# Performance work log

Measured on AMD Instinct MI355X. Metric: run time of the kernel, lower is better.

## Reference

```python
import jax, jax.numpy as jnp
import numpy as np

NUM_EMBEDDINGS = 1024
LATENT_SIZE = 256
N = 131072


def setup_inputs() -> dict:
    key = jax.random.key(0)
    k1, k2 = jax.random.split(key)
    inputs = jax.random.normal(k1, (N, LATENT_SIZE), dtype=jnp.float32)
    embed = jax.random.normal(k2, (LATENT_SIZE, NUM_EMBEDDINGS), dtype=jnp.float32)
    return {"inputs": inputs, "embed": embed}


def reference(inputs, embed):
    # Squared Euclidean distances: [N, K]
    dist = (
        jnp.sum(inputs * inputs, axis=1, keepdims=True)
        - 2.0 * (inputs @ embed)
        + jnp.sum(embed * embed, axis=0, keepdims=True)
    )
    embed_ind = jnp.argmin(dist, axis=1)  # [N]
    embed_onehot = jax.nn.one_hot(embed_ind, NUM_EMBEDDINGS, dtype=inputs.dtype)  # [N, K]
    # Gather codebook vectors: embedding lookup into embed.T -> [N, D]
    quantize = embed.T[embed_ind]
    # Commitment-style loss (eval path: no EMA buffer updates)
    loss = jnp.mean((jax.lax.stop_gradient(quantize) - inputs) ** 2)
    # Straight-through estimator
    quantize = inputs + jax.lax.stop_gradient(quantize - inputs)
    avg_probs = jnp.mean(embed_onehot, axis=0)  # [K]
    perplexity = jnp.exp(-jnp.sum(avg_probs * jnp.log(avg_probs + 1e-10)))
    return quantize, loss, perplexity, embed_ind
```

## Files before the change

### kernel.cpp

```cpp
#include <hip/hip_runtime.h>
#include <math.h>

#define M_ROWS 131072
#define D_DIM 256
#define NCODES 1024
#define QELEMS (M_ROWS * D_DIM)

#define WS_EMBEDT   0u
#define WS_ENORM    1048576u
#define WS_PARTIALS 1052672u
#define WS_COUNTS   9441280u
#define WS_LOSSP    9445376u
#define WS_IDX      9478144u

__global__ __launch_bounds__(256) void k_tnorm(const float* __restrict__ embed,
                                               float* __restrict__ embedT,
                                               float* __restrict__ enorm) {
  int c = blockIdx.x;
  int t = threadIdx.x;
  float v = embed[t * NCODES + c];
  embedT[c * D_DIM + t] = v;
  float s = v * v;
  for (int off = 32; off > 0; off >>= 1) s += __shfl_down(s, off, 64);
  __shared__ float red[4];
  if ((t & 63) == 0) red[t >> 6] = s;
  __syncthreads();
  if (t == 0) enorm[c] = red[0] + red[1] + red[2] + red[3];
}

__global__ __launch_bounds__(256, 2) void k_dist(const float* __restrict__ A,
                                                 const float* __restrict__ B,
                                                 const float* __restrict__ enorm,
                                                 float2* __restrict__ partials) {
  __shared__ float As[32][128];
  __shared__ float Bs[32][128];
  int bx = blockIdx.x;
  int ct = bx & 7;
  int rt = bx >> 3;
  int rowBase = rt * 128;
  int colBase = ct * 128;
  int t = threadIdx.x;
  int tx = t & 15;
  int ty = t >> 4;

  float acc[8][8];
#pragma unroll
  for (int i = 0; i < 8; ++i)
#pragma unroll
    for (int j = 0; j < 8; ++j) acc[i][j] = 0.f;

  for (int kc = 0; kc < 256; kc += 32) {
#pragma unroll
    for (int u = 0; u < 4; ++u) {
      int id = t + 256 * u;
      int r = id >> 3;
      int kq = id & 7;
      float4 v = *(const float4*)(A + (size_t)(rowBase + r) * D_DIM + kc + kq * 4);
      As[kq * 4 + 0][r] = v.x;
      As[kq * 4 + 1][r] = v.y;
      As[kq * 4 + 2][r] = v.z;
      As[kq * 4 + 3][r] = v.w;
    }
#pragma unroll
    for (int u = 0; u < 4; ++u) {
      int id = t + 256 * u;
      int k = id >> 5;
      int cq = id & 31;
      float4 v = *(const float4*)(B + (size_t)(kc + k) * NCODES + colBase + cq * 4);
      *(float4*)&Bs[k][cq * 4] = v;
    }
    __syncthreads();
#pragma unroll
    for (int k = 0; k < 32; ++k) {
      float a[8], b[8];
      *(float4*)&a[0] = *(const float4*)&As[k][ty * 4];
      *(float4*)&a[4] = *(const float4*)&As[k][64 + ty * 4];
      *(float4*)&b[0] = *(const float4*)&Bs[k][tx * 4];
      *(float4*)&b[4] = *(const float4*)&Bs[k][64 + tx * 4];
#pragma unroll
      for (int i = 0; i < 8; ++i)
#pragma unroll
        for (int j = 0; j < 8; ++j) acc[i][j] = fmaf(a[i], b[j], acc[i][j]);
    }
    __syncthreads();
  }

  float en[8];
#pragma unroll
  for (int j = 0; j < 4; ++j) {
    en[j] = enorm[colBase + tx * 4 + j];
    en[4 + j] = enorm[colBase + 64 + tx * 4 + j];
  }
#pragma unroll
  for (int s = 0; s < 8; ++s) {
    float best = 3.0e38f;
    int bidx = 0;
#pragma unroll
    for (int jj = 0; jj < 8; ++jj) {
      int c = colBase + (jj < 4 ? tx * 4 + jj : 64 + tx * 4 + (jj - 4));
      float d = fmaf(-2.f, acc[s][jj], en[jj]);
      if (d < best) { best = d; bidx = c; }
    }
    for (int off = 1; off < 16; off <<= 1) {
      float ob = __shfl_xor(best, off, 64);
      int oi = __shfl_xor(bidx, off, 64);
      if (ob < best || (ob == best && oi < bidx)) { best = ob; bidx = oi; }
    }
    if (tx == 0) {
      int grow = rowBase + (s < 4 ? ty * 4 + s : 64 + ty * 4 + (s - 4));
      partials[(size_t)grow * 8 + ct] = make_float2(best, (float)bidx);
    }
  }
}

__global__ __launch_bounds__(256) void k_argmin(const float2* __restrict__ partials,
                                                float* __restrict__ out_ind,
                                                int* __restrict__ idxbuf,
                                                int* __restrict__ counts) {
  int row = blockIdx.x * 256 + threadIdx.x;
  float best = 3.0e38f;
  int bi = 0;
#pragma unroll
  for (int tp = 0; tp < 8; ++tp) {
    float2 p = partials[(size_t)row * 8 + tp];
    int c = (int)p.y;
    if (p.x < best || (p.x == best && c < bi)) { best = p.x; bi = c; }
  }
  out_ind[row] = (float)bi;
  idxbuf[row] = bi;
  atomicAdd(&counts[bi], 1);
}

__global__ __launch_bounds__(256) void k_quant(const float* __restrict__ x,
                                               const float* __restrict__ embedT,
                                               const int* __restrict__ idxbuf,
                                               float* __restrict__ outq,
                                               float* __restrict__ lossPart) {
  int b = blockIdx.x;
  int t = threadIdx.x;
  int rlocal = t >> 6;
  int lane = t & 63;
  float s = 0.f;
#pragma unroll
  for (int ri = 0; ri < 4; ++ri) {
    int row = b * 16 + ri * 4 + rlocal;
    int idx = idxbuf[row];
    float4 xv = *(const float4*)(x + (size_t)row * D_DIM + lane * 4);
    float4 qv = *(const float4*)(embedT + (size_t)idx * D_DIM + lane * 4);
    float dx = qv.x - xv.x, dy = qv.y - xv.y, dz = qv.z - xv.z, dw = qv.w - xv.w;
    float4 o = make_float4(xv.x + dx, xv.y + dy, xv.z + dz, xv.w + dw);
    *(float4*)(outq + (size_t)row * D_DIM + lane * 4) = o;
    s = fmaf(dx, dx, s); s = fmaf(dy, dy, s); s = fmaf(dz, dz, s); s = fmaf(dw, dw, s);
  }
  for (int off = 32; off > 0; off >>= 1) s += __shfl_down(s, off, 64);
  __shared__ float red[4];
  if (lane == 0) red[rlocal] = s;
  __syncthreads();
  if (t == 0) lossPart[b] = red[0] + red[1] + red[2] + red[3];
}

__global__ __launch_bounds__(1024) void k_final(const int* __restrict__ counts,
                                                const float* __restrict__ lossPart,
                                                float* __restrict__ out_scalars) {
  int t = threadIdx.x;
  double ls = 0.0;
#pragma unroll
  for (int u = 0; u < 8; ++u) ls += (double)lossPart[t * 8 + u];
  float p = (float)counts[t] * (1.0f / (float)M_ROWS);
  float ent = p * logf(p + 1e-10f);
  double lred = ls;
  float ered = ent;
  for (int off = 32; off > 0; off >>= 1) {
    lred += __shfl_down(lred, off, 64);
    ered += __shfl_down(ered, off, 64);
  }
  __shared__ double lsh[16];
  __shared__ float esh[16];
  int w = t >> 6;
  if ((t & 63) == 0) { lsh[w] = lred; esh[w] = ered; }
  __syncthreads();
  if (t == 0) {
    double L = 0.0;
    float E = 0.f;
    for (int i = 0; i < 16; ++i) { L += lsh[i]; E += esh[i]; }
    out_scalars[0] = (float)(L / (double)QELEMS);
    out_scalars[1] = expf(-E);
  }
}

extern "C" void kernel_launch(void* const* d_in, const int* in_sizes, int n_in,
                              void* d_out, int out_size, void* d_ws, size_t ws_size,
                              hipStream_t stream) {
  const float* inputs = (const float*)d_in[0];
  const float* embed = (const float*)d_in[1];
  float* out = (float*)d_out;
  char* ws = (char*)d_ws;
  float* embedT = (float*)(ws + WS_EMBEDT);
  float* enorm = (float*)(ws + WS_ENORM);
  float2* partials = (float2*)(ws + WS_PARTIALS);
  int* counts = (int*)(ws + WS_COUNTS);
  float* lossPart = (float*)(ws + WS_LOSSP);
  int* idxbuf = (int*)(ws + WS_IDX);

  hipMemsetAsync(counts, 0, NCODES * sizeof(int), stream);
  k_tnorm<<<NCODES, 256, 0, stream>>>(embed, embedT, enorm);
  k_dist<<<8192, 256, 0, stream>>>(inputs, embed, enorm, partials);
  k_argmin<<<M_ROWS / 256, 256, 0, stream>>>(partials, out + QELEMS + 2, idxbuf, counts);
  k_quant<<<8192, 256, 0, stream>>>(inputs, embedT, idxbuf, out, lossPart);
  k_final<<<1, 1024, 0, stream>>>(counts, lossPart, out + QELEMS);
}
```

Before: 1.062 ms.

## Use split-bf16 MFMA for distance GEMM with top-2 exact rescoring

The FP32 FMA distance GEMM is replaced by MFMA bf16 instructions, with each operand split into hi and lo bf16 parts and three products accumulated to keep close to fp32 accuracy. The argmin path now tracks the top-2 candidates per row. The quant kernel recomputes exact fp32 distances for both candidates and picks the winner, which also moves the count atomics and index output there. This trades extra MFMA work, bf16 conversion in the load loop and a second gather row for much higher matrix throughput. The cost is some risk of argmin mismatches when the top two candidates are nearly tied.

```diff
diff --git a/kernel.cpp b/kernel.cpp
--- a/kernel.cpp
+++ b/kernel.cpp
@@ -6,20 +6,51 @@
 #define NCODES 1024
 #define QELEMS (M_ROWS * D_DIM)
 
+typedef __attribute__((ext_vector_type(4))) short short4v;
+typedef __attribute__((ext_vector_type(8))) short short8v;
+typedef __attribute__((ext_vector_type(4))) float f32x4;
+
 #define WS_EMBEDT   0u
-#define WS_ENORM    1048576u
-#define WS_PARTIALS 1052672u
-#define WS_COUNTS   9441280u
-#define WS_LOSSP    9445376u
-#define WS_IDX      9478144u
-
-__global__ __launch_bounds__(256) void k_tnorm(const float* __restrict__ embed,
-                                               float* __restrict__ embedT,
-                                               float* __restrict__ enorm) {
-  int c = blockIdx.x;
-  int t = threadIdx.x;
+#define WS_EHI      1048576u
+#define WS_ELO      1572864u
+#define WS_ENORM    2097152u
+#define WS_PART     2101248u
+#define WS_IDX2     18878464u
+#define WS_COUNTS   19927040u
+#define WS_LOSSP    19931136u
+
+__device__ inline unsigned short f2bf(float x) {
+  union { float f; unsigned u; } c; c.f = x;
+  unsigned u = c.u;
+  u += 0x7FFFu + ((u >> 16) & 1u);
+  return (unsigned short)(u >> 16);
+}
+__device__ inline float bf2f(unsigned short h) {
+  union { float f; unsigned u; } c; c.u = ((unsigned)h) << 16;
+  return c.f;
+}
+__device__ inline void merge2(float& b0, int& i0, float& b1, int& i1,
+                              float o0, int oi0, float o1, int oi1) {
+  if (o0 < b0 || (o0 == b0 && oi0 < i0)) {
+    if (b0 < o1 || (b0 == o1 && i0 < oi1)) { b1 = b0; i1 = i0; }
+    else { b1 = o1; i1 = oi1; }
+    b0 = o0; i0 = oi0;
+  } else {
+    if (o0 < b1 || (o0 == b1 && oi0 < i1)) { b1 = o0; i1 = oi0; }
+  }
+}
+
+__global__ __launch_bounds__(256) void k_prep(const float* __restrict__ embed,
+                                              float* __restrict__ embedT,
+                                              unsigned short* __restrict__ ehiT,
+                                              unsigned short* __restrict__ eloT,
+                                              float* __restrict__ enorm) {
+  int c = blockIdx.x, t = threadIdx.x;
   float v = embed[t * NCODES + c];
   embedT[c * D_DIM + t] = v;
+  unsigned short hi = f2bf(v);
+  ehiT[c * D_DIM + t] = hi;
+  eloT[c * D_DIM + t] = f2bf(v - bf2f(hi));
   float s = v * v;
   for (int off = 32; off > 0; off >>= 1) s += __shfl_down(s, off, 64);
   __shared__ float red[4];
@@ -28,133 +59,189 @@
   if (t == 0) enorm[c] = red[0] + red[1] + red[2] + red[3];
 }
 
-__global__ __launch_bounds__(256, 2) void k_dist(const float* __restrict__ A,
-                                                 const float* __restrict__ B,
+__global__ __launch_bounds__(256, 3) void k_dist(const float* __restrict__ A,
+                                                 const unsigned short* __restrict__ ehiT,
+                                                 const unsigned short* __restrict__ eloT,
                                                  const float* __restrict__ enorm,
-                                                 float2* __restrict__ partials) {
-  __shared__ float As[32][128];
-  __shared__ float Bs[32][128];
+                                                 float4* __restrict__ partials) {
+  __shared__ unsigned short sAhi[128 * 32];
+  __shared__ unsigned short sAlo[128 * 32];
+  __shared__ unsigned short sBhi[128 * 32];
+  __shared__ unsigned short sBlo[128 * 32];
+  __shared__ float4 sRed[2][128];
+
   int bx = blockIdx.x;
-  int ct = bx & 7;
-  int rt = bx >> 3;
-  int rowBase = rt * 128;
-  int colBase = ct * 128;
+  int ct = bx & 7, rt = bx >> 3;
+  int rowBase = rt << 7, colBase = ct << 7;
   int t = threadIdx.x;
-  int tx = t & 15;
-  int ty = t >> 4;
-
-  float acc[8][8];
-#pragma unroll
-  for (int i = 0; i < 8; ++i)
-#pragma unroll
-    for (int j = 0; j < 8; ++j) acc[i][j] = 0.f;
-
-  for (int kc = 0; kc < 256; kc += 32) {
+  int w = t >> 6, lane = t & 63;
+  int wr = w >> 1, wc = w & 1;
+  int lm = lane & 15, quad = lane >> 4;
+
+  int sr = t >> 1;
+  int skh = (t & 1) << 4;
+
+  f32x4 acc[4][4];
+#pragma unroll
+  for (int i = 0; i < 4; ++i)
+#pragma unroll
+    for (int j = 0; j < 4; ++j) acc[i][j] = (f32x4){0.f, 0.f, 0.f, 0.f};
+
+  int aoff[4], boff[4];
+#pragma unroll
+  for (int ti = 0; ti < 4; ++ti) {
+    int r = (wr << 6) + (ti << 4) + lm;
+    aoff[ti] = r * 32 + ((quad ^ (r & 3)) << 3);
+    int n = (wc << 6) + (ti << 4) + lm;
+    boff[ti] = n * 32 + ((quad ^ (n & 3)) << 3);
+  }
+
+  const float* Arow = A + (size_t)(rowBase + sr) * D_DIM + skh;
+  const unsigned short* Bhirow = ehiT + (size_t)(colBase + sr) * D_DIM + skh;
+  const unsigned short* Blorow = eloT + (size_t)(colBase + sr) * D_DIM + skh;
+
+  for (int kc = 0; kc < D_DIM; kc += 32) {
 #pragma unroll
     for (int u = 0; u < 4; ++u) {
-      int id = t + 256 * u;
-      int r = id >> 3;
-      int kq = id & 7;
-      float4 v = *(const float4*)(A + (size_t)(rowBase + r) * D_DIM + kc + kq * 4);
-      As[kq * 4 + 0][r] = v.x;
-      As[kq * 4 + 1][r] = v.y;
-      As[kq * 4 + 2][r] = v.z;
-      As[kq * 4 + 3][r] = v.w;
-    }
-#pragma unroll
-    for (int u = 0; u < 4; ++u) {
-      int id = t + 256 * u;
-      int k = id >> 5;
-      int cq = id & 31;
-      float4 v = *(const float4*)(B + (size_t)(kc + k) * NCODES + colBase + cq * 4);
-      *(float4*)&Bs[k][cq * 4] = v;
+      float4 v = *(const float4*)(Arow + kc + (u << 2));
+      int koff = skh + (u << 2);
+      int dst = sr * 32 + (((koff >> 3) ^ (sr & 3)) << 3) + (koff & 7);
+      unsigned short h0 = f2bf(v.x), h1 = f2bf(v.y), h2 = f2bf(v.z), h3 = f2bf(v.w);
+      short4v hv = {(short)h0, (short)h1, (short)h2, (short)h3};
+      *(short4v*)&sAhi[dst] = hv;
+      short4v lv = {(short)f2bf(v.x - bf2f(h0)), (short)f2bf(v.y - bf2f(h1)),
+                    (short)f2bf(v.z - bf2f(h2)), (short)f2bf(v.w - bf2f(h3))};
+      *(short4v*)&sAlo[dst] = lv;
+    }
+#pragma unroll
+    for (int h = 0; h < 2; ++h) {
+      int koff = skh + (h << 3);
+      int dst = sr * 32 + (((koff >> 3) ^ (sr & 3)) << 3);
+      *(uint4*)&sBhi[dst] = *(const uint4*)(Bhirow + kc + (h << 3));
+      *(uint4*)&sBlo[dst] = *(const uint4*)(Blorow + kc + (h << 3));
     }
     __syncthreads();
-#pragma unroll
-    for (int k = 0; k < 32; ++k) {
-      float a[8], b[8];
-      *(float4*)&a[0] = *(const float4*)&As[k][ty * 4];
-      *(float4*)&a[4] = *(const float4*)&As[k][64 + ty * 4];
-      *(float4*)&b[0] = *(const float4*)&Bs[k][tx * 4];
-      *(float4*)&b[4] = *(const float4*)&Bs[k][64 + tx * 4];
-#pragma unroll
-      for (int i = 0; i < 8; ++i)
-#pragma unroll
-        for (int j = 0; j < 8; ++j) acc[i][j] = fmaf(a[i], b[j], acc[i][j]);
-    }
+
+    short8v ahi[4], alo[4], bhi[4], blo[4];
+#pragma unroll
+    for (int i = 0; i < 4; ++i) {
+      ahi[i] = *(const short8v*)&sAhi[aoff[i]];
+      bhi[i] = *(const short8v*)&sBhi[boff[i]];
+      blo[i] = *(const short8v*)&sBlo[boff[i]];
+      alo[i] = *(const short8v*)&sAlo[aoff[i]];
+    }
+#pragma unroll
+    for (int i = 0; i < 4; ++i)
+#pragma unroll
+      for (int j = 0; j < 4; ++j)
+        acc[i][j] = __builtin_amdgcn_mfma_f32_16x16x32_bf16(ahi[i], bhi[j], acc[i][j], 0, 0, 0);
+#pragma unroll
+    for (int i = 0; i < 4; ++i)
+#pragma unroll
+      for (int j = 0; j < 4; ++j)
+        acc[i][j] = __builtin_amdgcn_mfma_f32_16x16x32_bf16(ahi[i], blo[j], acc[i][j], 0, 0, 0);
+#pragma unroll
+    for (int i = 0; i < 4; ++i)
+#pragma unroll
+      for (int j = 0; j < 4; ++j)
+        acc[i][j] = __builtin_amdgcn_mfma_f32_16x16x32_bf16(alo[i], bhi[j], acc[i][j], 0, 0, 0);
     __syncthreads();
   }
 
-  float en[8];
+  float enC[4]; int cidx[4];
 #pragma unroll
   for (int j = 0; j < 4; ++j) {
-    en[j] = enorm[colBase + tx * 4 + j];
-    en[4 + j] = enorm[colBase + 64 + tx * 4 + j];
-  }
-#pragma unroll
-  for (int s = 0; s < 8; ++s) {
-    float best = 3.0e38f;
-    int bidx = 0;
-#pragma unroll
-    for (int jj = 0; jj < 8; ++jj) {
-      int c = colBase + (jj < 4 ? tx * 4 + jj : 64 + tx * 4 + (jj - 4));
-      float d = fmaf(-2.f, acc[s][jj], en[jj]);
-      if (d < best) { best = d; bidx = c; }
-    }
-    for (int off = 1; off < 16; off <<= 1) {
-      float ob = __shfl_xor(best, off, 64);
-      int oi = __shfl_xor(bidx, off, 64);
-      if (ob < best || (ob == best && oi < bidx)) { best = ob; bidx = oi; }
-    }
-    if (tx == 0) {
-      int grow = rowBase + (s < 4 ? ty * 4 + s : 64 + ty * 4 + (s - 4));
-      partials[(size_t)grow * 8 + ct] = make_float2(best, (float)bidx);
-    }
-  }
-}
-
-__global__ __launch_bounds__(256) void k_argmin(const float2* __restrict__ partials,
-                                                float* __restrict__ out_ind,
-                                                int* __restrict__ idxbuf,
-                                                int* __restrict__ counts) {
+    cidx[j] = colBase + (wc << 6) + (j << 4) + lm;
+    enC[j] = enorm[cidx[j]];
+  }
+#pragma unroll
+  for (int ti = 0; ti < 4; ++ti) {
+#pragma unroll
+    for (int reg = 0; reg < 4; ++reg) {
+      float b0 = 3.0e38f, b1 = 3.0e38f;
+      int i0 = 0x7fffffff, i1 = 0x7fffffff;
+#pragma unroll
+      for (int j = 0; j < 4; ++j) {
+        float v = fmaf(-2.f, acc[ti][j][reg], enC[j]);
+        int c = cidx[j];
+        if (v < b0 || (v == b0 && c < i0)) { b1 = b0; i1 = i0; b0 = v; i0 = c; }
+        else if (v < b1 || (v == b1 && c < i1)) { b1 = v; i1 = c; }
+      }
+      for (int m = 1; m < 16; m <<= 1) {
+        float o0 = __shfl_xor(b0, m, 64); int oi0 = __shfl_xor(i0, m, 64);
+        float o1 = __shfl_xor(b1, m, 64); int oi1 = __shfl_xor(i1, m, 64);
+        merge2(b0, i0, b1, i1, o0, oi0, o1, oi1);
+      }
+      if (lm == 0) {
+        int rloc = (wr << 6) + (ti << 4) + (quad << 2) + reg;
+        sRed[wc][rloc] = make_float4(b0, (float)i0, b1, (float)i1);
+      }
+    }
+  }
+  __syncthreads();
+  if (t < 128) {
+    float4 p = sRed[0][t];
+    float b0 = p.x; int i0 = (int)p.y; float b1 = p.z; int i1 = (int)p.w;
+    float4 q = sRed[1][t];
+    merge2(b0, i0, b1, i1, q.x, (int)q.y, q.z, (int)q.w);
+    partials[(size_t)ct * M_ROWS + rowBase + t] = make_float4(b0, (float)i0, b1, (float)i1);
+  }
+}
+
+__global__ __launch_bounds__(256) void k_argmin(const float4* __restrict__ partials,
+                                                int2* __restrict__ idx2) {
   int row = blockIdx.x * 256 + threadIdx.x;
-  float best = 3.0e38f;
-  int bi = 0;
+  float b0 = 3.0e38f, b1 = 3.0e38f;
+  int i0 = 0x7fffffff, i1 = 0x7fffffff;
 #pragma unroll
   for (int tp = 0; tp < 8; ++tp) {
-    float2 p = partials[(size_t)row * 8 + tp];
-    int c = (int)p.y;
-    if (p.x < best || (p.x == best && c < bi)) { best = p.x; bi = c; }
-  }
-  out_ind[row] = (float)bi;
-  idxbuf[row] = bi;
-  atomicAdd(&counts[bi], 1);
+    float4 p = partials[(size_t)tp * M_ROWS + row];
+    merge2(b0, i0, b1, i1, p.x, (int)p.y, p.z, (int)p.w);
+  }
+  idx2[row] = make_int2(i0, i1);
 }
 
 __global__ __launch_bounds__(256) void k_quant(const float* __restrict__ x,
                                                const float* __restrict__ embedT,
-                                               const int* __restrict__ idxbuf,
+                                               const int2* __restrict__ idx2,
                                                float* __restrict__ outq,
+                                               float* __restrict__ out_ind,
+                                               int* __restrict__ counts,
                                                float* __restrict__ lossPart) {
-  int b = blockIdx.x;
-  int t = threadIdx.x;
-  int rlocal = t >> 6;
-  int lane = t & 63;
-  float s = 0.f;
+  int b = blockIdx.x, t = threadIdx.x;
+  int rl = t >> 6, lane = t & 63;
+  float lsum = 0.f;
+  __shared__ float red[4];
 #pragma unroll
   for (int ri = 0; ri < 4; ++ri) {
-    int row = b * 16 + ri * 4 + rlocal;
-    int idx = idxbuf[row];
-    float4 xv = *(const float4*)(x + (size_t)row * D_DIM + lane * 4);
-    float4 qv = *(const float4*)(embedT + (size_t)idx * D_DIM + lane * 4);
-    float dx = qv.x - xv.x, dy = qv.y - xv.y, dz = qv.z - xv.z, dw = qv.w - xv.w;
-    float4 o = make_float4(xv.x + dx, xv.y + dy, xv.z + dz, xv.w + dw);
-    *(float4*)(outq + (size_t)row * D_DIM + lane * 4) = o;
-    s = fmaf(dx, dx, s); s = fmaf(dy, dy, s); s = fmaf(dz, dz, s); s = fmaf(dw, dw, s);
-  }
-  for (int off = 32; off > 0; off >>= 1) s += __shfl_down(s, off, 64);
-  __shared__ float red[4];
-  if (lane == 0) red[rlocal] = s;
+    int row = b * 16 + ri * 4 + rl;
+    int2 cc = idx2[row];
+    float4 xv = *(const float4*)(x + (size_t)row * D_DIM + (lane << 2));
+    float4 q0 = *(const float4*)(embedT + (size_t)cc.x * D_DIM + (lane << 2));
+    float4 q1 = *(const float4*)(embedT + (size_t)cc.y * D_DIM + (lane << 2));
+    float a0 = q0.x - xv.x, a1 = q0.y - xv.y, a2 = q0.z - xv.z, a3 = q0.w - xv.w;
+    float c0 = q1.x - xv.x, c1 = q1.y - xv.y, c2 = q1.z - xv.z, c3 = q1.w - xv.w;
+    float d0 = fmaf(a0, a0, fmaf(a1, a1, fmaf(a2, a2, a3 * a3)));
+    float d1 = fmaf(c0, c0, fmaf(c1, c1, fmaf(c2, c2, c3 * c3)));
+    for (int m = 1; m < 64; m <<= 1) {
+      d0 += __shfl_xor(d0, m, 64);
+      d1 += __shfl_xor(d1, m, 64);
+    }
+    bool sel = (d1 < d0) || (d1 == d0 && cc.y < cc.x);
+    int widx = sel ? cc.y : cc.x;
+    float4 qv;
+    qv.x = sel ? q1.x : q0.x; qv.y = sel ? q1.y : q0.y;
+    qv.z = sel ? q1.z : q0.z; qv.w = sel ? q1.w : q0.w;
+    float4 o = make_float4(xv.x + (qv.x - xv.x), xv.y + (qv.y - xv.y),
+                           xv.z + (qv.z - xv.z), xv.w + (qv.w - xv.w));
+    *(float4*)(outq + (size_t)row * D_DIM + (lane << 2)) = o;
+    lsum += sel ? d1 : d0;
+    if (lane == 0) {
+      out_ind[row] = (float)widx;
+      atomicAdd(&counts[widx], 1);
+    }
+  }
+  if (lane == 0) red[rl] = lsum;
   __syncthreads();
   if (t == 0) lossPart[b] = red[0] + red[1] + red[2] + red[3];
 }
@@ -196,16 +283,19 @@
   float* out = (float*)d_out;
   char* ws = (char*)d_ws;
   float* embedT = (float*)(ws + WS_EMBEDT);
+  unsigned short* ehiT = (unsigned short*)(ws + WS_EHI);
+  unsigned short* eloT = (unsigned short*)(ws + WS_ELO);
   float* enorm = (float*)(ws + WS_ENORM);
-  float2* partials = (float2*)(ws + WS_PARTIALS);
+  float4* partials = (float4*)(ws + WS_PART);
+  int2* idx2 = (int2*)(ws + WS_IDX2);
   int* counts = (int*)(ws + WS_COUNTS);
   float* lossPart = (float*)(ws + WS_LOSSP);
-  int* idxbuf = (int*)(ws + WS_IDX);
 
   hipMemsetAsync(counts, 0, NCODES * sizeof(int), stream);
-  k_tnorm<<<NCODES, 256, 0, stream>>>(embed, embedT, enorm);
-  k_dist<<<8192, 256, 0, stream>>>(inputs, embed, enorm, partials);
-  k_argmin<<<M_ROWS / 256, 256, 0, stream>>>(partials, out + QELEMS + 2, idxbuf, counts);
-  k_quant<<<8192, 256, 0, stream>>>(inputs, embedT, idxbuf, out, lossPart);
+  k_prep<<<NCODES, 256, 0, stream>>>(embed, embedT, ehiT, eloT, enorm);
+  k_dist<<<8192, 256, 0, stream>>>(inputs, ehiT, eloT, enorm, partials);
+  k_argmin<<<M_ROWS / 256, 256, 0, stream>>>(partials, idx2);
+  k_quant<<<8192, 256, 0, stream>>>(inputs, embedT, idx2, out, out + QELEMS + 2,
+                                    counts, lossPart);
   k_final<<<1, 1024, 0, stream>>>(counts, lossPart, out + QELEMS);
 }
```

Measured after the change: 972.5 us. -8.4%, faster.
